# Kernel optimization log

Measured on AMD Instinct MI355X. Metric: run time of the kernel, lower is better.

The kernel has to match this reference:

```python
import jax, jax.numpy as jnp
import numpy as np

N_EMB = 512
DIM = 64
BETA = 0.25
EPS = 1e-10


def setup_inputs() -> dict:
    key = jax.random.key(0)
    k1, k2 = jax.random.split(key)
    z = jax.random.normal(k1, (32, 64, 64, 64), dtype=jnp.float32)  # (B, C=DIM, H, W)
    # embedding weight initialized uniform(-1/K, 1/K) as in the module
    weight = jax.random.uniform(k2, (N_EMB, DIM), dtype=jnp.float32,
                                minval=-1.0 / N_EMB, maxval=1.0 / N_EMB)
    return {"z": z, "weight": weight}


def reference(z, weight):
    # (B,C,H,W) -> (B,H,W,C)
    zp = jnp.transpose(z, (0, 2, 3, 1))
    zf = zp.reshape(-1, DIM)  # (N, D)
    # pairwise squared distances ||z||^2 + ||e||^2 - 2 z.e  -> (N, K)
    d = (jnp.sum(zf * zf, axis=1, keepdims=True)
         + jnp.sum(weight * weight, axis=1)
         - 2.0 * zf @ weight.T)
    codebook = jnp.argmin(d, axis=1)  # (N,)
    encodings = jax.nn.one_hot(codebook, N_EMB, dtype=zf.dtype)  # (N, K)
    # direct gather == one_hot @ weight (same math, efficient form)
    z_q = weight[codebook].reshape(zp.shape)
    sg = jax.lax.stop_gradient
    loss = jnp.mean((sg(z_q) - zp) ** 2) + BETA * jnp.mean((z_q - sg(zp)) ** 2)
    # straight-through estimator
    z_q = zp + sg(z_q - zp)
    e_mean = jnp.mean(encodings, axis=0)
    perplexity = jnp.exp(-jnp.sum(e_mean * jnp.log(e_mean + EPS)))
    z_q = jnp.transpose(z_q, (0, 3, 1, 2))  # back to (B,C,H,W)
    return (loss, z_q, perplexity, encodings, codebook)
```

## Files before the change

### kernel.cpp

```cpp
#include <hip/hip_runtime.h>
#include <math.h>

#define NK 512
#define DIMV 64
#define NPTS (32*64*64)
#define NELEM (32*64*64*64)
#define WT_STRIDE 132

#define OFF_LOSS 0
#define OFF_ZQ   1
#define OFF_PERP (1 + NELEM)
#define OFF_ENC  (2 + NELEM)
#define OFF_CB   (2 + NELEM + (size_t)NPTS * NK)

__global__ __launch_bounds__(256) void vq_main(const float* __restrict__ zg,
                                               const float* __restrict__ wg,
                                               float* __restrict__ out,
                                               int* __restrict__ hist,
                                               double* __restrict__ lossAcc) {
    const int t = threadIdx.x;
    const int blk = blockIdx.x;
    const int b = blk >> 6;
    const int h = blk & 63;

    __shared__ __align__(16) float zt[64 * 64];
    __shared__ __align__(16) float wt[64 * WT_STRIDE];
    __shared__ float aRow[64];
    __shared__ float bnd[128];
    __shared__ int   idxs[64];
    __shared__ float rsum[256];

    float* zqt  = wt;
    float* redv = wt + 4096;
    int*   redi = (int*)(wt + 4096 + 16 * 66);

    {
        const int w = t & 63;
        const int c0 = t >> 6;
        const size_t base = (size_t)b * 262144 + (size_t)h * 64;
        #pragma unroll
        for (int c = c0; c < 64; c += 4)
            zt[c * 64 + w] = zg[base + (size_t)c * 4096 + w];
    }
    __syncthreads();

    if (t < 64) {
        float s = 0.f;
        for (int d = 0; d < 64; ++d) {
            float v = zt[d * 64 + t];
            s = __fadd_rn(s, __fmul_rn(v, v));
        }
        aRow[t] = s;
    }
    __syncthreads();

    const int tx = t & 15;
    const int ty = t >> 4;
    const int ty4 = ty * 4;
    const int tx8 = tx * 8;

    float av[4];
    #pragma unroll
    for (int i = 0; i < 4; ++i) av[i] = aRow[ty4 + i];

    float best[4];
    int bidx[4];
    #pragma unroll
    for (int i = 0; i < 4; ++i) { best[i] = INFINITY; bidx[i] = 0; }

    for (int chunk = 0; chunk < 4; ++chunk) {
        {
            const int d = t & 63, kk0 = t >> 6;
            #pragma unroll
            for (int kk = kk0; kk < 128; kk += 4)
                wt[d * WT_STRIDE + kk] = wg[((size_t)(chunk * 128 + kk)) * 64 + d];
        }
        __syncthreads();

        if (t < 128) {
            float s = 0.f;
            for (int d = 0; d < 64; ++d) {
                float v = wt[d * WT_STRIDE + t];
                s = __fadd_rn(s, __fmul_rn(v, v));
            }
            bnd[t] = s;
        }
        __syncthreads();

        float acc[4][8];
        #pragma unroll
        for (int i = 0; i < 4; ++i)
            #pragma unroll
            for (int j = 0; j < 8; ++j) acc[i][j] = 0.f;

        const float* ztp = zt + ty4;
        const float* wtp = wt + tx8;
        #pragma unroll 4
        for (int d = 0; d < 64; ++d) {
            const float4 zv = *(const float4*)(ztp + d * 64);
            const float4 w0 = *(const float4*)(wtp + d * WT_STRIDE);
            const float4 w1 = *(const float4*)(wtp + d * WT_STRIDE + 4);
            const float zr[4] = {zv.x, zv.y, zv.z, zv.w};
            const float wr[8] = {w0.x, w0.y, w0.z, w0.w, w1.x, w1.y, w1.z, w1.w};
            #pragma unroll
            for (int i = 0; i < 4; ++i)
                #pragma unroll
                for (int j = 0; j < 8; ++j)
                    acc[i][j] = fmaf(zr[i], wr[j], acc[i][j]);
        }

        #pragma unroll
        for (int i = 0; i < 4; ++i) {
            #pragma unroll
            for (int j = 0; j < 8; ++j) {
                float dist = __fsub_rn(__fadd_rn(av[i], bnd[tx8 + j]), 2.0f * acc[i][j]);
                int k = chunk * 128 + tx8 + j;
                if (dist < best[i]) { best[i] = dist; bidx[i] = k; }
            }
        }
        __syncthreads();
    }

    #pragma unroll
    for (int i = 0; i < 4; ++i) {
        redv[tx * 66 + ty4 + i] = best[i];
        redi[tx * 64 + ty4 + i] = bidx[i];
    }
    __syncthreads();

    if (t < 64) {
        float bv = redv[t];
        int bi = redi[t];
        #pragma unroll
        for (int x = 1; x < 16; ++x) {
            float v = redv[x * 66 + t];
            int ii = redi[x * 64 + t];
            if (v < bv || (v == bv && ii < bi)) { bv = v; bi = ii; }
        }
        idxs[t] = bi;
        atomicAdd(&hist[bi], 1);
        out[OFF_CB + (size_t)blk * 64 + t] = (float)bi;
        const float4* wr4 = (const float4*)(wg + (size_t)bi * 64);
        #pragma unroll
        for (int q = 0; q < 16; ++q) {
            float4 v = wr4[q];
            zqt[(4 * q + 0) * 64 + t] = v.x;
            zqt[(4 * q + 1) * 64 + t] = v.y;
            zqt[(4 * q + 2) * 64 + t] = v.z;
            zqt[(4 * q + 3) * 64 + t] = v.w;
        }
    }
    __syncthreads();

    {
        float4* enc = (float4*)(out + OFF_ENC + (size_t)blk * 64 * NK);
        for (int e = t; e < 64 * 128; e += 256) {
            int r = e >> 7, c4 = e & 127;
            int idx = idxs[r];
            float4 v = make_float4(0.f, 0.f, 0.f, 0.f);
            if ((idx >> 2) == c4) ((float*)&v)[idx & 3] = 1.0f;
            enc[(size_t)r * 128 + c4] = v;
        }
    }

    float lsum = 0.f;
    {
        float* zq = out + OFF_ZQ + (size_t)b * 262144 + (size_t)h * 64;
        for (int e = t; e < 4096; e += 256) {
            int p = e & 63, d = e >> 6;
            float zv = zt[d * 64 + p];
            float qv = zqt[d * 64 + p];
            float diff = __fsub_rn(qv, zv);
            lsum = __fadd_rn(lsum, __fmul_rn(diff, diff));
            zq[(size_t)d * 4096 + p] = __fadd_rn(zv, diff);
        }
    }
    rsum[t] = lsum;
    __syncthreads();
    for (int s = 128; s > 0; s >>= 1) {
        if (t < s) rsum[t] += rsum[t + s];
        __syncthreads();
    }
    if (t == 0) atomicAdd(lossAcc, (double)rsum[0]);
}

__global__ __launch_bounds__(512) void vq_finalize(const int* __restrict__ hist,
                                                   const double* __restrict__ lossAcc,
                                                   float* __restrict__ out) {
    __shared__ float sh[512];
    const int t = threadIdx.x;
    float p = (float)hist[t] / (float)NPTS;
    sh[t] = __fmul_rn(p, logf(__fadd_rn(p, 1e-10f)));
    __syncthreads();
    for (int s = 256; s > 0; s >>= 1) {
        if (t < s) sh[t] += sh[t + s];
        __syncthreads();
    }
    if (t == 0) {
        float m = (float)(*lossAcc / (double)NELEM);
        out[OFF_LOSS] = __fadd_rn(m, __fmul_rn(0.25f, m));
        out[OFF_PERP] = expf(-sh[0]);
    }
}

extern "C" void kernel_launch(void* const* d_in, const int* in_sizes, int n_in,
                              void* d_out, int out_size, void* d_ws, size_t ws_size,
                              hipStream_t stream) {
    const float* z = (const float*)d_in[0];
    const float* w = (const float*)d_in[1];
    float* out = (float*)d_out;
    int* hist = (int*)d_ws;
    double* lossAcc = (double*)((char*)d_ws + 2048);

    hipMemsetAsync(d_ws, 0, 4096, stream);
    vq_main<<<2048, 256, 0, stream>>>(z, w, out, hist, lossAcc);
    vq_finalize<<<1, 512, 0, stream>>>(hist, lossAcc, out);
}
```

Baseline: 472.1 us.

## Restructure VQ kernel: per-lane z in registers, pre-transposed codebook with uniform loads

A small prep kernel transposes the codebook into an interleaved [k/8][d][8] layout and precomputes codebook norms. The main kernel then gives each wave one spatial row and half the codebook. Each lane keeps its 64-dim z vector in registers, and the codebook values are wave-uniform reads that can become scalar loads. This drops the per-block shared-memory codebook staging, its barriers and the redundant norm recomputation, and replaces the block-wide loss reduction with a shuffle reduction. It raises register pressure (64 z floats plus accumulators), and each z element now costs eight FMAs per codebook load instead of using a shared-memory register-tiled GEMM.

```diff
diff --git a/kernel.cpp b/kernel.cpp
--- a/kernel.cpp
+++ b/kernel.cpp
@@ -2,10 +2,8 @@
 #include <math.h>
 
 #define NK 512
-#define DIMV 64
 #define NPTS (32*64*64)
 #define NELEM (32*64*64*64)
-#define WT_STRIDE 132
 
 #define OFF_LOSS 0
 #define OFF_ZQ   1
@@ -13,175 +11,162 @@
 #define OFF_ENC  (2 + NELEM)
 #define OFF_CB   (2 + NELEM + (size_t)NPTS * NK)
 
-__global__ __launch_bounds__(256) void vq_main(const float* __restrict__ zg,
-                                               const float* __restrict__ wg,
-                                               float* __restrict__ out,
-                                               int* __restrict__ hist,
-                                               double* __restrict__ lossAcc) {
+
+__global__ __launch_bounds__(256) void vq_prep(const float* __restrict__ wg,
+                                               float* __restrict__ wTT,
+                                               float* __restrict__ bnd) {
+    __shared__ float tl[64 * 65];
     const int t = threadIdx.x;
-    const int blk = blockIdx.x;
-    const int b = blk >> 6;
-    const int h = blk & 63;
-
-    __shared__ __align__(16) float zt[64 * 64];
-    __shared__ __align__(16) float wt[64 * WT_STRIDE];
-    __shared__ float aRow[64];
-    __shared__ float bnd[128];
-    __shared__ int   idxs[64];
-    __shared__ float rsum[256];
-
-    float* zqt  = wt;
-    float* redv = wt + 4096;
-    int*   redi = (int*)(wt + 4096 + 16 * 66);
-
-    {
-        const int w = t & 63;
-        const int c0 = t >> 6;
-        const size_t base = (size_t)b * 262144 + (size_t)h * 64;
-        #pragma unroll
-        for (int c = c0; c < 64; c += 4)
-            zt[c * 64 + w] = zg[base + (size_t)c * 4096 + w];
-    }
-    __syncthreads();
-
+    const int kbase = blockIdx.x * 64;
+    #pragma unroll
+    for (int it = 0; it < 16; ++it) {
+        int i = it * 256 + t;
+        int k = i >> 6, d = i & 63;
+        tl[k * 65 + d] = wg[(size_t)(kbase + k) * 64 + d];
+    }
+    __syncthreads();
+    #pragma unroll
+    for (int it = 0; it < 16; ++it) {
+        int i = it * 256 + t;
+        int kk = i & 63, d = i >> 6;
+        int k = kbase + kk;
+        wTT[(size_t)((k >> 3) * 64 + d) * 8 + (k & 7)] = tl[kk * 65 + d];
+    }
     if (t < 64) {
         float s = 0.f;
-        for (int d = 0; d < 64; ++d) {
-            float v = zt[d * 64 + t];
-            s = __fadd_rn(s, __fmul_rn(v, v));
-        }
-        aRow[t] = s;
-    }
-    __syncthreads();
-
-    const int tx = t & 15;
-    const int ty = t >> 4;
-    const int ty4 = ty * 4;
-    const int tx8 = tx * 8;
-
-    float av[4];
-    #pragma unroll
-    for (int i = 0; i < 4; ++i) av[i] = aRow[ty4 + i];
-
-    float best[4];
-    int bidx[4];
-    #pragma unroll
-    for (int i = 0; i < 4; ++i) { best[i] = INFINITY; bidx[i] = 0; }
-
-    for (int chunk = 0; chunk < 4; ++chunk) {
-        {
-            const int d = t & 63, kk0 = t >> 6;
-            #pragma unroll
-            for (int kk = kk0; kk < 128; kk += 4)
-                wt[d * WT_STRIDE + kk] = wg[((size_t)(chunk * 128 + kk)) * 64 + d];
-        }
-        __syncthreads();
-
-        if (t < 128) {
-            float s = 0.f;
-            for (int d = 0; d < 64; ++d) {
-                float v = wt[d * WT_STRIDE + t];
-                s = __fadd_rn(s, __fmul_rn(v, v));
-            }
-            bnd[t] = s;
-        }
-        __syncthreads();
-
-        float acc[4][8];
-        #pragma unroll
-        for (int i = 0; i < 4; ++i)
-            #pragma unroll
-            for (int j = 0; j < 8; ++j) acc[i][j] = 0.f;
-
-        const float* ztp = zt + ty4;
-        const float* wtp = wt + tx8;
         #pragma unroll 4
         for (int d = 0; d < 64; ++d) {
-            const float4 zv = *(const float4*)(ztp + d * 64);
-            const float4 w0 = *(const float4*)(wtp + d * WT_STRIDE);
-            const float4 w1 = *(const float4*)(wtp + d * WT_STRIDE + 4);
-            const float zr[4] = {zv.x, zv.y, zv.z, zv.w};
-            const float wr[8] = {w0.x, w0.y, w0.z, w0.w, w1.x, w1.y, w1.z, w1.w};
+            float v = tl[t * 65 + d];
+            s = __fadd_rn(s, __fmul_rn(v, v));
+        }
+        bnd[kbase + t] = s;
+    }
+}
+
+__global__ __launch_bounds__(256, 4) void vq_fused(const float* __restrict__ zg,
+                                                   const float* __restrict__ wg,
+                                                   const float* __restrict__ wTT,
+                                                   const float* __restrict__ bndg,
+                                                   float* __restrict__ out,
+                                                   int* __restrict__ hist,
+                                                   double* __restrict__ lossAcc) {
+    const int t = threadIdx.x;
+    const int wave = t >> 6;
+    const int lane = t & 63;
+    const int rowInBlk = wave >> 1;
+    const int half = wave & 1;
+    const int r = blockIdx.x * 2 + rowInBlk;
+    const int b = r >> 6;
+    const int h = r & 63;
+    const size_t base = (size_t)b * 262144 + (size_t)h * 64;
+
+    __shared__ float shv[4][64];
+    __shared__ int   shi[4][64];
+    __shared__ int   shm[2][64];
+
+    float zreg[64];
+    #pragma unroll
+    for (int d = 0; d < 64; ++d)
+        zreg[d] = zg[base + (size_t)d * 4096 + lane];
+
+    float a = 0.f;
+    #pragma unroll
+    for (int d = 0; d < 64; ++d)
+        a = __fadd_rn(a, __fmul_rn(zreg[d], zreg[d]));
+
+    const int shalf = __builtin_amdgcn_readfirstlane(half);
+    const float* wbase = wTT + (size_t)shalf * 32 * 512;
+    const float* bnb = bndg + shalf * 256;
+
+    float best = INFINITY;
+    int bidx = 0;
+
+    #pragma unroll 1
+    for (int cc = 0; cc < 32; ++cc) {
+        const float* wrow = wbase + cc * 512;
+        float acc[8];
+        #pragma unroll
+        for (int j = 0; j < 8; ++j) acc[j] = 0.f;
+
+        #pragma unroll
+        for (int d = 0; d < 64; ++d) {
+            const float zv = zreg[d];
             #pragma unroll
-            for (int i = 0; i < 4; ++i)
-                #pragma unroll
-                for (int j = 0; j < 8; ++j)
-                    acc[i][j] = fmaf(zr[i], wr[j], acc[i][j]);
-        }
-
-        #pragma unroll
-        for (int i = 0; i < 4; ++i) {
-            #pragma unroll
-            for (int j = 0; j < 8; ++j) {
-                float dist = __fsub_rn(__fadd_rn(av[i], bnd[tx8 + j]), 2.0f * acc[i][j]);
-                int k = chunk * 128 + tx8 + j;
-                if (dist < best[i]) { best[i] = dist; bidx[i] = k; }
-            }
-        }
-        __syncthreads();
-    }
-
-    #pragma unroll
-    for (int i = 0; i < 4; ++i) {
-        redv[tx * 66 + ty4 + i] = best[i];
-        redi[tx * 64 + ty4 + i] = bidx[i];
-    }
-    __syncthreads();
-
-    if (t < 64) {
-        float bv = redv[t];
-        int bi = redi[t];
-        #pragma unroll
-        for (int x = 1; x < 16; ++x) {
-            float v = redv[x * 66 + t];
-            int ii = redi[x * 64 + t];
-            if (v < bv || (v == bv && ii < bi)) { bv = v; bi = ii; }
-        }
-        idxs[t] = bi;
-        atomicAdd(&hist[bi], 1);
-        out[OFF_CB + (size_t)blk * 64 + t] = (float)bi;
-        const float4* wr4 = (const float4*)(wg + (size_t)bi * 64);
-        #pragma unroll
-        for (int q = 0; q < 16; ++q) {
-            float4 v = wr4[q];
-            zqt[(4 * q + 0) * 64 + t] = v.x;
-            zqt[(4 * q + 1) * 64 + t] = v.y;
-            zqt[(4 * q + 2) * 64 + t] = v.z;
-            zqt[(4 * q + 3) * 64 + t] = v.w;
-        }
+            for (int j = 0; j < 8; ++j)
+                acc[j] = fmaf(zv, wrow[d * 8 + j], acc[j]);
+        }
+
+        #pragma unroll
+        for (int j = 0; j < 8; ++j) {
+            float dist = __fsub_rn(__fadd_rn(a, bnb[cc * 8 + j]), 2.0f * acc[j]);
+            int k = shalf * 256 + cc * 8 + j;
+            if (dist < best) { best = dist; bidx = k; }
+        }
+    }
+
+    shv[wave][lane] = best;
+    shi[wave][lane] = bidx;
+    __syncthreads();
+    const int w0 = rowInBlk * 2;
+    float v0 = shv[w0][lane];     int i0 = shi[w0][lane];
+    float v1 = shv[w0 + 1][lane]; int i1 = shi[w0 + 1][lane];
+    const int mi = (v1 < v0) ? i1 : i0;
+
+    if (half == 0) {
+        shm[rowInBlk][lane] = mi;
+        out[OFF_CB + (size_t)r * 64 + lane] = (float)mi;
+        atomicAdd(&hist[mi], 1);
     }
     __syncthreads();
 
     {
-        float4* enc = (float4*)(out + OFF_ENC + (size_t)blk * 64 * NK);
-        for (int e = t; e < 64 * 128; e += 256) {
-            int r = e >> 7, c4 = e & 127;
-            int idx = idxs[r];
-            float4 v = make_float4(0.f, 0.f, 0.f, 0.f);
-            if ((idx >> 2) == c4) ((float*)&v)[idx & 3] = 1.0f;
-            enc[(size_t)r * 128 + c4] = v;
+        float* encb = out + OFF_ENC + ((size_t)r * 64) * 512;
+        const int e0 = lane * 4;
+        #pragma unroll 4
+        for (int p = 0; p < 32; ++p) {
+            int pt = shalf * 32 + p;
+            int idx = shm[rowInBlk][pt];
+            float* erow = encb + (size_t)pt * 512;
+            float4 A, B;
+            A.x = (e0 + 0 == idx) ? 1.f : 0.f;
+            A.y = (e0 + 1 == idx) ? 1.f : 0.f;
+            A.z = (e0 + 2 == idx) ? 1.f : 0.f;
+            A.w = (e0 + 3 == idx) ? 1.f : 0.f;
+            B.x = (e0 + 256 == idx) ? 1.f : 0.f;
+            B.y = (e0 + 257 == idx) ? 1.f : 0.f;
+            B.z = (e0 + 258 == idx) ? 1.f : 0.f;
+            B.w = (e0 + 259 == idx) ? 1.f : 0.f;
+            *(float4*)(erow + e0) = A;
+            *(float4*)(erow + 256 + e0) = B;
         }
     }
 
     float lsum = 0.f;
     {
-        float* zq = out + OFF_ZQ + (size_t)b * 262144 + (size_t)h * 64;
-        for (int e = t; e < 4096; e += 256) {
-            int p = e & 63, d = e >> 6;
-            float zv = zt[d * 64 + p];
-            float qv = zqt[d * 64 + p];
-            float diff = __fsub_rn(qv, zv);
+        const int dlo = shalf * 32;
+        const float4* wr4 = (const float4*)(wg + (size_t)mi * 64 + dlo);
+        float q[32];
+        #pragma unroll
+        for (int e = 0; e < 8; ++e) {
+            float4 v = wr4[e];
+            q[4 * e + 0] = v.x; q[4 * e + 1] = v.y;
+            q[4 * e + 2] = v.z; q[4 * e + 3] = v.w;
+        }
+        float* zq = out + OFF_ZQ + base;
+        #pragma unroll
+        for (int dd = 0; dd < 32; ++dd) {
+            int d = dlo + dd;
+            float zv = zreg[d];
+            float diff = __fsub_rn(q[dd], zv);
             lsum = __fadd_rn(lsum, __fmul_rn(diff, diff));
-            zq[(size_t)d * 4096 + p] = __fadd_rn(zv, diff);
-        }
-    }
-    rsum[t] = lsum;
-    __syncthreads();
-    for (int s = 128; s > 0; s >>= 1) {
-        if (t < s) rsum[t] += rsum[t + s];
-        __syncthreads();
-    }
-    if (t == 0) atomicAdd(lossAcc, (double)rsum[0]);
+            zq[(size_t)d * 4096 + lane] = __fadd_rn(zv, diff);
+        }
+    }
+    #pragma unroll
+    for (int off = 32; off > 0; off >>= 1)
+        lsum += __shfl_down(lsum, off);
+    if (lane == 0)
+        atomicAdd(lossAcc, (double)lsum);
 }
 
 __global__ __launch_bounds__(512) void vq_finalize(const int* __restrict__ hist,
@@ -211,8 +196,11 @@
     float* out = (float*)d_out;
     int* hist = (int*)d_ws;
     double* lossAcc = (double*)((char*)d_ws + 2048);
-
-    hipMemsetAsync(d_ws, 0, 4096, stream);
-    vq_main<<<2048, 256, 0, stream>>>(z, w, out, hist, lossAcc);
+    float* wTT = (float*)((char*)d_ws + 4096);
+    float* bnd = wTT + 64 * 512;
+
+    (void)hipMemsetAsync(d_ws, 0, 4096, stream);
+    vq_prep<<<8, 256, 0, stream>>>(w, wTT, bnd);
+    vq_fused<<<1024, 256, 0, stream>>>(z, w, wTT, bnd, out, hist, lossAcc);
     vq_finalize<<<1, 512, 0, stream>>>(hist, lossAcc, out);
 }
```

Measured after the change: 505.1 us. 1.07x slower.
